# Kernel tuning notes

Measured on AMD Instinct MI355X. Metric: run time of the kernel, lower is better.

Reference implementation:

```python
import jax, jax.numpy as jnp
import numpy as np

B, N, C, F, E, K = 2, 2048, 1024, 4096, 8, 2

def setup_inputs() -> dict:
    key = jax.random.key(0)
    k = jax.random.split(key, 6)
    xavier1 = float(np.sqrt(6.0 / (C + F)))
    xavier2 = float(np.sqrt(6.0 / (F + C)))
    return {
        "x": jax.random.normal(k[0], (B, N, C), dtype=jnp.float32),
        "router_w": jax.random.normal(k[1], (E, C), dtype=jnp.float32) * 0.01,
        "w1": jax.random.uniform(k[2], (E, F, C), dtype=jnp.float32, minval=-xavier1, maxval=xavier1),
        "b1": jnp.zeros((E, F), dtype=jnp.float32),
        "w2": jax.random.uniform(k[3], (E, C, F), dtype=jnp.float32, minval=-xavier2, maxval=xavier2),
        "b2": jnp.zeros((E, C), dtype=jnp.float32),
    }

def reference(x, router_w, w1, b1, w2, b2):
    Bb, Nn, Cc = x.shape
    x_flat = x.reshape(-1, Cc)                                   # [T, C]
    # Router (eval mode: no noise)
    logits = jnp.einsum('tc,ec->te', x_flat, router_w)           # [T, E]
    probs = jax.nn.softmax(logits, axis=-1)
    top_w, top_idx = jax.lax.top_k(probs, K)                     # [T, K]
    top_w = top_w / (jnp.sum(top_w, axis=-1, keepdims=True) + 1e-9)
    # Dense all-expert MLP (same math as the per-expert gather/scatter loop)
    h = jnp.einsum('tc,efc->tef', x_flat, w1) + b1[None]          # [T, E, F]
    h = jax.nn.relu(h)
    y = jnp.einsum('tef,ecf->tec', h, w2) + b2[None]              # [T, E, C]
    # Gather the K selected experts per token and combine
    sel = jnp.take_along_axis(y, top_idx[:, :, None], axis=1)    # [T, K, C]
    out = jnp.einsum('tkc,tk->tc', sel, top_w)                   # [T, C]
    return out.reshape(Bb, Nn, Cc)
```

## Files before the change

kernel.cpp:

```cpp
#include <hip/hip_runtime.h>
#include <hip/hip_fp16.h>


#define T_TOK 4096
#define C_DIM 1024
#define F_DIM 4096
#define E_NUM 8
#define MAXT 80
#define NP   (MAXT * 128)
#define SUB_H 4096

typedef float f32x4 __attribute__((ext_vector_type(4)));
typedef _Float16 half8 __attribute__((ext_vector_type(8)));
typedef _Float16 half4 __attribute__((ext_vector_type(4)));

#define AS1 __attribute__((address_space(1)))
#define AS3 __attribute__((address_space(3)))

__device__ __forceinline__ half8 cvt8(float4 f0, float4 f1) {
  half8 hv;
  hv[0] = (_Float16)f0.x; hv[1] = (_Float16)f0.y; hv[2] = (_Float16)f0.z; hv[3] = (_Float16)f0.w;
  hv[4] = (_Float16)f1.x; hv[5] = (_Float16)f1.y; hv[6] = (_Float16)f1.z; hv[7] = (_Float16)f1.w;
  return hv;
}

__device__ __forceinline__ int xcd_swz(int bid, int nwg) {
  int xcd = bid & 7, rest = bid >> 3;
  int q = nwg >> 3, r = nwg & 7;
  return (xcd < r ? xcd * (q + 1) : r * (q + 1) + (xcd - r) * q) + rest;
}

__global__ __launch_bounds__(256) void router_kernel(
    const float* __restrict__ x, const float* __restrict__ rw,
    int* __restrict__ top_idx, float* __restrict__ top_w)
{
  int t = blockIdx.x * 4 + (threadIdx.x >> 6);
  int lane = threadIdx.x & 63;
  const float* xr = x + (size_t)t * C_DIM;
  float acc[E_NUM];
#pragma unroll
  for (int e = 0; e < E_NUM; ++e) acc[e] = 0.f;
  for (int j = 0; j < C_DIM / 64; ++j) {
    int c = j * 64 + lane;
    float xv = xr[c];
#pragma unroll
    for (int e = 0; e < E_NUM; ++e) acc[e] += xv * rw[e * C_DIM + c];
  }
#pragma unroll
  for (int e = 0; e < E_NUM; ++e) {
    float v = acc[e];
#pragma unroll
    for (int off = 32; off > 0; off >>= 1) v += __shfl_xor(v, off);
    acc[e] = v;
  }
  if (lane == 0) {
    float mx = acc[0];
    for (int e = 1; e < E_NUM; ++e) mx = fmaxf(mx, acc[e]);
    float p[E_NUM]; float Z = 0.f;
    for (int e = 0; e < E_NUM; ++e) { p[e] = expf(acc[e] - mx); Z += p[e]; }
    int b0 = 0;
    for (int e = 1; e < E_NUM; ++e) if (p[e] > p[b0]) b0 = e;
    int b1i = -1; float pb = -1.f;
    for (int e = 0; e < E_NUM; ++e) if (e != b0 && p[e] > pb) { pb = p[e]; b1i = e; }
    float p0 = p[b0] / Z, p1 = pb / Z;
    float s = p0 + p1 + 1e-9f;
    top_idx[t * 2 + 0] = b0;
    top_idx[t * 2 + 1] = b1i;
    top_w[t * 2 + 0] = p0 / s;
    top_w[t * 2 + 1] = p1 / s;
  }
}

__global__ void build_lists(const int* __restrict__ top_idx,
                            int* __restrict__ rows_g, int* __restrict__ counts,
                            int* __restrict__ tile_off, int* __restrict__ inv)
{
  int e = threadIdx.x >> 6;
  int lane = threadIdx.x & 63;
  int cnt = 0;
  for (int t0 = 0; t0 < T_TOK; t0 += 64) {
    int t = t0 + lane;
    bool sel = (top_idx[t * 2] == e) || (top_idx[t * 2 + 1] == e);
    cnt += __popcll(__ballot(sel));
  }
  if (lane == 0) counts[e] = cnt;
  __syncthreads();
  if (threadIdx.x == 0) {
    int o = 0;
    for (int i = 0; i < E_NUM; ++i) { tile_off[i] = o; o += 2 * ((counts[i] + 255) >> 8); }
    tile_off[E_NUM] = o;
  }
  __syncthreads();
  int base = tile_off[e] * 128;
  int pos = 0;
  for (int t0 = 0; t0 < T_TOK; t0 += 64) {
    int t = t0 + lane;
    int i0 = top_idx[t * 2], i1 = top_idx[t * 2 + 1];
    bool sel = (i0 == e) || (i1 == e);
    unsigned long long mask = __ballot(sel);
    if (sel) {
      int p = pos + __popcll(mask & ((1ull << lane) - 1ull));
      int slot = t * 2 + ((i0 == e) ? 0 : 1);
      rows_g[base + p] = slot;
      inv[slot] = (e << 16) | (base + p);
    }
    pos += __popcll(mask);
  }
}

__global__ __launch_bounds__(256) void gather_x(
    const float* __restrict__ x, const int* __restrict__ rows_g,
    const int* __restrict__ counts, const int* __restrict__ tile_off,
    _Float16* __restrict__ xg)
{
  unsigned g = blockIdx.x * 256 + threadIdx.x;
  unsigned p = g >> 7, ccr = g & 127;
  int gt = p >> 7, r = p & 127;
  int kc32 = ccr >> 2, c4d = ccr & 3;
  int c4s = c4d ^ (r & 3);
  int e = -1;
#pragma unroll
  for (int i = 0; i < E_NUM; ++i)
    if (gt >= tile_off[i] && gt < tile_off[i + 1]) e = i;
  half8 hv = {};
  if (e >= 0) {
    int nrem = counts[e] - (gt - tile_off[e]) * 128;
    if (r < nrem) {
      int t = rows_g[p] >> 1;
      const float4* s = reinterpret_cast<const float4*>(
          x + (size_t)t * C_DIM + kc32 * 32 + c4s * 8);
      hv = cvt8(s[0], s[1]);
    }
  }
  *reinterpret_cast<half8*>(xg + ((size_t)gt * 32 + kc32) * SUB_H + r * 32 + (c4d << 3)) = hv;
}

__global__ __launch_bounds__(256) void cvt_w(
    const float* __restrict__ w1, const float* __restrict__ w2,
    _Float16* __restrict__ w1t, _Float16* __restrict__ w2t,
    int ch, int Fc, int lgnftl, int lgnkc32, unsigned halfChunks)
{
  unsigned g = blockIdx.x * 256 + threadIdx.x;
  if (g < halfChunks) {
    unsigned tile = g >> 9;
    unsigned kc32 = tile & 31;
    unsigned et = tile >> 5;
    unsigned ftl = et & ((1u << lgnftl) - 1);
    unsigned e = et >> lgnftl;
    unsigned r = (g >> 2) & 127;
    unsigned sc = g & 3;
    unsigned c4s = sc ^ (r & 3);
    unsigned frow = ftl * 128 + r;
    const float4* s = reinterpret_cast<const float4*>(
        w1 + ((size_t)e * F_DIM + ch * Fc + frow) * C_DIM + kc32 * 32 + c4s * 8);
    *reinterpret_cast<half8*>(w1t + (size_t)g * 8) = cvt8(s[0], s[1]);
  } else {
    unsigned g2 = g - halfChunks;
    unsigned tile = g2 >> 9;
    unsigned kc32 = tile & ((1u << lgnkc32) - 1);
    unsigned et = tile >> lgnkc32;
    unsigned ct = et & 7;
    unsigned e = et >> 3;
    unsigned r = (g2 >> 2) & 127;
    unsigned sc = g2 & 3;
    unsigned c4s = sc ^ (r & 3);
    unsigned c = ct * 128 + r;
    const float4* s = reinterpret_cast<const float4*>(
        w2 + ((size_t)e * C_DIM + c) * F_DIM + ch * Fc + kc32 * 32 + c4s * 8);
    *reinterpret_cast<half8*>(w2t + (size_t)g2 * 8) = cvt8(s[0], s[1]);
  }
}

#define STAGE32(slot_, a0_, a1_, b0_, b1_)                                        \
  {                                                                               \
    int o_ = tid * 8;                                                             \
    __builtin_amdgcn_global_load_lds((const AS1 void*)((a0_) + o_),               \
        (AS3 void*)(lds + ((slot_) * 4 + 0) * SUB_H + o_), 16, 0, 0);             \
    __builtin_amdgcn_global_load_lds((const AS1 void*)((a1_) + o_),               \
        (AS3 void*)(lds + ((slot_) * 4 + 1) * SUB_H + o_), 16, 0, 0);             \
    __builtin_amdgcn_global_load_lds((const AS1 void*)((b0_) + o_),               \
        (AS3 void*)(lds + ((slot_) * 4 + 2) * SUB_H + o_), 16, 0, 0);             \
    __builtin_amdgcn_global_load_lds((const AS1 void*)((b1_) + o_),               \
        (AS3 void*)(lds + ((slot_) * 4 + 3) * SUB_H + o_), 16, 0, 0);             \
  }

#define COMPUTE32(slot_)                                                          \
  {                                                                               \
    const _Float16* aT_ = lds + (size_t)((slot_) * 4 + wr) * SUB_H;               \
    const _Float16* bT_ = lds + (size_t)((slot_) * 4 + 2 + (wc >> 1)) * SUB_H;    \
    const int c4_ = lane >> 4;                                                    \
    half8 aF[8], bF[4];                                                           \
    _Pragma("unroll")                                                             \
    for (int m = 0; m < 8; ++m) {                                                 \
      int r = m * 16 + (lane & 15);                                               \
      aF[m] = *reinterpret_cast<const half8*>(&aT_[r * 32 + ((c4_ ^ (r & 3)) << 3)]); \
    }                                                                             \
    _Pragma("unroll")                                                             \
    for (int n = 0; n < 4; ++n) {                                                 \
      int rb = (wc & 1) * 64 + n * 16 + (lane & 15);                              \
      bF[n] = *reinterpret_cast<const half8*>(&bT_[rb * 32 + ((c4_ ^ (rb & 3)) << 3)]); \
    }                                                                             \
    _Pragma("unroll")                                                             \
    for (int m = 0; m < 8; ++m)                                                   \
      _Pragma("unroll")                                                           \
      for (int n = 0; n < 4; ++n)                                                 \
        acc[m][n] = __builtin_amdgcn_mfma_f32_16x16x32_f16(bF[n], aF[m], acc[m][n], 0, 0, 0); \
  }

#define WAIT_BAR(cnt_)                                                            \
  asm volatile("s_waitcnt vmcnt(" #cnt_ ")" ::: "memory");                        \
  __builtin_amdgcn_sched_barrier(0);                                              \
  __builtin_amdgcn_s_barrier();                                                   \
  __builtin_amdgcn_sched_barrier(0);

#define KLOOP(n_)                                                                 \
  STAGE32(0, At0, At1, Bt0, Bt1);                                                 \
  STAGE32(1, At0 + SUB_H, At1 + SUB_H, Bt0 + SUB_H, Bt1 + SUB_H);                 \
  STAGE32(2, At0 + 2 * SUB_H, At1 + 2 * SUB_H, Bt0 + 2 * SUB_H, Bt1 + 2 * SUB_H); \
  for (int s = 0; s < (n_) - 2; ++s) {                                            \
    WAIT_BAR(8);                                                                  \
    COMPUTE32(s & 3);                                                             \
    if (s + 3 < (n_)) {                                                           \
      size_t ko_ = (size_t)(s + 3) * SUB_H;                                       \
      STAGE32((s + 3) & 3, At0 + ko_, At1 + ko_, Bt0 + ko_, Bt1 + ko_);           \
    }                                                                             \
  }                                                                               \
  WAIT_BAR(4);                                                                    \
  COMPUTE32(((n_) - 2) & 3);                                                      \
  WAIT_BAR(0);                                                                    \
  COMPUTE32(((n_) - 1) & 3);

__global__ __launch_bounds__(512, 2) void gemm1_kernel(
    const _Float16* __restrict__ xg, const _Float16* __restrict__ w1t,
    const float* __restrict__ b1, const int* __restrict__ tile_off,
    _Float16* __restrict__ ht, int ch, int Fc)
{
  extern __shared__ _Float16 lds[];
  const int NFT = Fc >> 8;
  const int GBf = (NFT < 4) ? NFT : 4;
  const int perg = 8 * GBf;
  const int ngrpF = NFT / GBf;
  const int wgid = xcd_swz(blockIdx.x, gridDim.x);
  const int grp = wgid / perg;
  const int inner = wgid - grp * perg;
  const int ftq = inner % GBf;
  const int gp = inner / GBf;
  const int gtg = grp / ngrpF;
  const int ftg = grp - gtg * ngrpF;
  const int ft = ftg * GBf + ftq;
  const int gt = (gtg * 8 + gp) * 2;
  if (gt >= tile_off[E_NUM]) return;
  int e = 0;
  while (gt >= tile_off[e + 1]) ++e;
  const int nftl = Fc >> 7;
  const _Float16* At0 = xg + (size_t)gt * 32 * SUB_H;
  const _Float16* At1 = xg + (size_t)(gt + 1) * 32 * SUB_H;
  const _Float16* Bt0 = w1t + (size_t)(e * nftl + 2 * ft) * 32 * SUB_H;
  const _Float16* Bt1 = w1t + (size_t)(e * nftl + 2 * ft + 1) * 32 * SUB_H;

  const int tid = threadIdx.x;
  const int lane = tid & 63;
  const int wave = tid >> 6;
  const int wr = wave >> 2, wc = wave & 3;

  f32x4 acc[8][4];
#pragma unroll
  for (int m = 0; m < 8; ++m)
#pragma unroll
    for (int n = 0; n < 4; ++n) acc[m][n] = (f32x4){0.f, 0.f, 0.f, 0.f};

  KLOOP(32);

  const int nkc32F = Fc >> 5;
  const int gtw = gt + wr;
  const float* b1e = b1 + e * F_DIM + ch * Fc;
#pragma unroll
  for (int m = 0; m < 8; ++m) {
    int tok = m * 16 + (lane & 15);
#pragma unroll
    for (int n = 0; n < 4; ++n) {
      int flb = ft * 256 + wc * 64 + n * 16 + ((lane >> 4) << 2);
      float4 bv = *reinterpret_cast<const float4*>(b1e + flb);
      half4 hv;
      hv[0] = (_Float16)fmaxf(acc[m][n][0] + bv.x, 0.f);
      hv[1] = (_Float16)fmaxf(acc[m][n][1] + bv.y, 0.f);
      hv[2] = (_Float16)fmaxf(acc[m][n][2] + bv.z, 0.f);
      hv[3] = (_Float16)fmaxf(acc[m][n][3] + bv.w, 0.f);
      *reinterpret_cast<half4*>(
          ht + ((size_t)gtw * nkc32F + (flb >> 5)) * SUB_H + tok * 32 +
          (((((flb >> 3) & 3) ^ (tok & 3))) << 3) + (flb & 7)) = hv;
    }
  }
}

__global__ __launch_bounds__(512, 2) void gemm2_kernel(
    const _Float16* __restrict__ ht, const _Float16* __restrict__ w2t,
    const int* __restrict__ tile_off, _Float16* __restrict__ y,
    int Fc, int kspl, int accum)
{
  extern __shared__ _Float16 lds[];
  const int NGT2 = MAXT / 2;
  const int wgid = xcd_swz(blockIdx.x, gridDim.x);
  const int ks = wgid / (NGT2 * 4);
  const int r0 = wgid - ks * NGT2 * 4;
  const int grp8 = r0 >> 5;
  const int inner = r0 & 31;
  const int ct2 = inner & 3;
  const int gp = inner >> 2;
  const int gt = (grp8 * 8 + gp) * 2;
  if (gt >= tile_off[E_NUM]) return;
  int e = 0;
  while (gt >= tile_off[e + 1]) ++e;
  const int nkc32 = Fc >> 5;
  const int klen = nkc32 / kspl;
  const _Float16* At0 = ht + ((size_t)gt * nkc32 + ks * klen) * SUB_H;
  const _Float16* At1 = ht + ((size_t)(gt + 1) * nkc32 + ks * klen) * SUB_H;
  const _Float16* Bt0 = w2t + ((size_t)(e * 8 + 2 * ct2) * nkc32 + ks * klen) * SUB_H;
  const _Float16* Bt1 = w2t + ((size_t)(e * 8 + 2 * ct2 + 1) * nkc32 + ks * klen) * SUB_H;

  const int tid = threadIdx.x;
  const int lane = tid & 63;
  const int wave = tid >> 6;
  const int wr = wave >> 2, wc = wave & 3;

  f32x4 acc[8][4];
#pragma unroll
  for (int m = 0; m < 8; ++m)
#pragma unroll
    for (int n = 0; n < 4; ++n) acc[m][n] = (f32x4){0.f, 0.f, 0.f, 0.f};

  KLOOP(klen);

  _Float16* yk = y + ((size_t)(ks * MAXT + gt + wr) * 128) * C_DIM;
#pragma unroll
  for (int m = 0; m < 8; ++m) {
    int tok = m * 16 + (lane & 15);
#pragma unroll
    for (int n = 0; n < 4; ++n) {
      int cb = ct2 * 256 + wc * 64 + n * 16 + ((lane >> 4) << 2);
      half4* p = reinterpret_cast<half4*>(yk + (size_t)tok * C_DIM + cb);
      half4 hv;
      if (accum) {
        half4 old = *p;
        hv[0] = (_Float16)(acc[m][n][0] + (float)old[0]);
        hv[1] = (_Float16)(acc[m][n][1] + (float)old[1]);
        hv[2] = (_Float16)(acc[m][n][2] + (float)old[2]);
        hv[3] = (_Float16)(acc[m][n][3] + (float)old[3]);
      } else {
        hv[0] = (_Float16)acc[m][n][0];
        hv[1] = (_Float16)acc[m][n][1];
        hv[2] = (_Float16)acc[m][n][2];
        hv[3] = (_Float16)acc[m][n][3];
      }
      *p = hv;
    }
  }
}

__global__ __launch_bounds__(256) void combine_kernel(
    const _Float16* __restrict__ y, const int* __restrict__ inv,
    const float* __restrict__ top_w, const float* __restrict__ b2,
    float* __restrict__ out, int kspl)
{
  int g = blockIdx.x * 256 + threadIdx.x;
  int t = g >> 7, c8 = (g & 127) << 3;
  float o[8];
#pragma unroll
  for (int i = 0; i < 8; ++i) o[i] = 0.f;
#pragma unroll
  for (int k = 0; k < 2; ++k) {
    int iv = inv[t * 2 + k];
    int e = iv >> 16, pos = iv & 0xffff;
    float w = top_w[t * 2 + k];
    const float4* bb = reinterpret_cast<const float4*>(b2 + e * C_DIM + c8);
    float4 bv0 = bb[0], bv1 = bb[1];
    float s[8] = {bv0.x, bv0.y, bv0.z, bv0.w, bv1.x, bv1.y, bv1.z, bv1.w};
    for (int ks = 0; ks < kspl; ++ks) {
      half8 hv = *reinterpret_cast<const half8*>(
          y + ((size_t)(ks * MAXT * 128 + pos)) * C_DIM + c8);
#pragma unroll
      for (int i = 0; i < 8; ++i) s[i] += (float)hv[i];
    }
#pragma unroll
    for (int i = 0; i < 8; ++i) o[i] += w * s[i];
  }
  float4* op = reinterpret_cast<float4*>(out + (size_t)t * C_DIM + c8);
  op[0] = (float4){o[0], o[1], o[2], o[3]};
  op[1] = (float4){o[4], o[5], o[6], o[7]};
}

extern "C" void kernel_launch(void* const* d_in, const int* in_sizes, int n_in,
                              void* d_out, int out_size, void* d_ws, size_t ws_size,
                              hipStream_t stream)
{
  const float* x  = (const float*)d_in[0];
  const float* rw = (const float*)d_in[1];
  const float* w1 = (const float*)d_in[2];
  const float* b1 = (const float*)d_in[3];
  const float* w2 = (const float*)d_in[4];
  const float* b2 = (const float*)d_in[5];
  float* out = (float*)d_out;

  char* ws = (char*)d_ws;
  size_t off = 0;
  auto carve = [&](size_t bytes) -> void* {
    void* p = ws + off;
    off += (bytes + 255) & ~(size_t)255;
    return p;
  };
  int*   top_idx  = (int*)carve((size_t)T_TOK * 2 * sizeof(int));
  float* top_w    = (float*)carve((size_t)T_TOK * 2 * sizeof(float));
  int*   counts   = (int*)carve(E_NUM * sizeof(int));
  int*   tile_off = (int*)carve((E_NUM + 1) * sizeof(int));
  int*   rows_g   = (int*)carve((size_t)NP * sizeof(int));
  int*   inv      = (int*)carve((size_t)T_TOK * 2 * sizeof(int));
  _Float16* xg    = (_Float16*)carve((size_t)MAXT * 32 * SUB_H * sizeof(_Float16));
  _Float16* y     = (_Float16*)carve((size_t)4 * NP * C_DIM * sizeof(_Float16));
  size_t fixed = off;

  int nchunk = 8;
  const int cands[4] = {1, 2, 4, 8};
  for (int ci = 0; ci < 4; ++ci) {
    int n = cands[ci];
    size_t fc = (size_t)(F_DIM / n);
    size_t w1b = ((size_t)E_NUM * fc * C_DIM * 2 + 255) & ~(size_t)255;
    size_t w2b = ((size_t)E_NUM * C_DIM * fc * 2 + 255) & ~(size_t)255;
    size_t htb = ((size_t)MAXT * (fc >> 5) * SUB_H * 2 + 255) & ~(size_t)255;
    if (fixed + w1b + w2b + htb <= ws_size) { nchunk = n; break; }
  }
  const int Fc = F_DIM / nchunk;
  int lgFc = 0; while ((1 << lgFc) < Fc) ++lgFc;
  _Float16* w1t = (_Float16*)carve((size_t)E_NUM * Fc * C_DIM * sizeof(_Float16));
  _Float16* w2t = (_Float16*)carve((size_t)E_NUM * C_DIM * Fc * sizeof(_Float16));
  _Float16* ht  = (_Float16*)carve((size_t)MAXT * (Fc >> 5) * SUB_H * sizeof(_Float16));

  const int kspl = (Fc >= 2048) ? 4 : 2;
  const size_t dynLds = (size_t)16 * SUB_H * sizeof(_Float16);

  router_kernel<<<T_TOK / 4, 256, 0, stream>>>(x, rw, top_idx, top_w);
  build_lists<<<1, 512, 0, stream>>>(top_idx, rows_g, counts, tile_off, inv);
  gather_x<<<(MAXT * 128 * 128) / 256, 256, 0, stream>>>(x, rows_g, counts, tile_off, xg);

  const unsigned halfChunks = (unsigned)Fc << 10;
  for (int ch = 0; ch < nchunk; ++ch) {
    cvt_w<<<8 * Fc, 256, 0, stream>>>(w1, w2, w1t, w2t, ch, Fc, lgFc - 7, lgFc - 5, halfChunks);
    gemm1_kernel<<<(MAXT / 2) * (Fc / 256), 512, dynLds, stream>>>(
        xg, w1t, b1, tile_off, ht, ch, Fc);
    gemm2_kernel<<<(MAXT / 2) * 4 * kspl, 512, dynLds, stream>>>(
        ht, w2t, tile_off, y, Fc, kspl, ch != 0);
  }
  combine_kernel<<<(T_TOK * 128) / 256, 256, 0, stream>>>(y, inv, top_w, b2, out, kspl);
}
```

Before: 358.7 us.

## Re-swizzle LDS tiles to 64-row XOR layout and split K-step into ping-pong halves

Changes the packed fp16 tile layout for activations, hidden states and weights from a 32-wide row with a 2-bit XOR swizzle to a 64-wide row with a 3-bit XOR swizzle, to cut LDS bank conflicts on fragment reads. Each K step of the GEMM main loop is now split into two halves that interleave LDS fragment reads, split global-to-LDS issues, and 16-MFMA groups run at raised wave priority, separated by extra barriers. The goal is better overlap of LDS reads with MFMA work and lower register pressure from holding only half the A fragments at a time. The cost is more barriers per K step. Every producer and consumer must agree on the new layout.

```diff
diff --git a/kernel.cpp b/kernel.cpp
--- a/kernel.cpp
+++ b/kernel.cpp
@@ -114,10 +114,9 @@
     _Float16* __restrict__ xg)
 {
   unsigned g = blockIdx.x * 256 + threadIdx.x;
-  unsigned p = g >> 7, ccr = g & 127;
+  unsigned p = g >> 7, c8g = g & 127;
   int gt = p >> 7, r = p & 127;
-  int kc32 = ccr >> 2, c4d = ccr & 3;
-  int c4s = c4d ^ (r & 3);
+  int ks32 = c8g >> 2, kidx = c8g & 3;
   int e = -1;
 #pragma unroll
   for (int i = 0; i < E_NUM; ++i)
@@ -128,107 +127,131 @@
     if (r < nrem) {
       int t = rows_g[p] >> 1;
       const float4* s = reinterpret_cast<const float4*>(
-          x + (size_t)t * C_DIM + kc32 * 32 + c4s * 8);
+          x + (size_t)t * C_DIM + ks32 * 32 + kidx * 8);
       hv = cvt8(s[0], s[1]);
     }
   }
-  *reinterpret_cast<half8*>(xg + ((size_t)gt * 32 + kc32) * SUB_H + r * 32 + (c4d << 3)) = hv;
+  int q = r & 63, h = r >> 6;
+  int slot = ((h << 2) | kidx) ^ (q & 7);
+  *reinterpret_cast<half8*>(
+      xg + ((size_t)gt * 32 + ks32) * SUB_H + q * 64 + slot * 8) = hv;
 }
 
 __global__ __launch_bounds__(256) void cvt_w(
     const float* __restrict__ w1, const float* __restrict__ w2,
     _Float16* __restrict__ w1t, _Float16* __restrict__ w2t,
-    int ch, int Fc, int lgnftl, int lgnkc32, unsigned halfChunks)
+    int ch, int Fc, int lgnftl, int lgnfs32, unsigned halfChunks)
 {
   unsigned g = blockIdx.x * 256 + threadIdx.x;
   if (g < halfChunks) {
     unsigned tile = g >> 9;
-    unsigned kc32 = tile & 31;
+    unsigned ks32 = tile & 31;
     unsigned et = tile >> 5;
     unsigned ftl = et & ((1u << lgnftl) - 1);
     unsigned e = et >> lgnftl;
-    unsigned r = (g >> 2) & 127;
-    unsigned sc = g & 3;
-    unsigned c4s = sc ^ (r & 3);
+    unsigned c = g & 511;
+    unsigned q = c >> 3, slot = c & 7;
+    unsigned sl = slot ^ (q & 7);
+    unsigned h = sl >> 2, kidx = sl & 3;
+    unsigned r = h * 64 + q;
     unsigned frow = ftl * 128 + r;
     const float4* s = reinterpret_cast<const float4*>(
-        w1 + ((size_t)e * F_DIM + ch * Fc + frow) * C_DIM + kc32 * 32 + c4s * 8);
+        w1 + ((size_t)e * F_DIM + ch * Fc + frow) * C_DIM + ks32 * 32 + kidx * 8);
     *reinterpret_cast<half8*>(w1t + (size_t)g * 8) = cvt8(s[0], s[1]);
   } else {
     unsigned g2 = g - halfChunks;
     unsigned tile = g2 >> 9;
-    unsigned kc32 = tile & ((1u << lgnkc32) - 1);
-    unsigned et = tile >> lgnkc32;
+    unsigned fs32 = tile & ((1u << lgnfs32) - 1);
+    unsigned et = tile >> lgnfs32;
     unsigned ct = et & 7;
     unsigned e = et >> 3;
-    unsigned r = (g2 >> 2) & 127;
-    unsigned sc = g2 & 3;
-    unsigned c4s = sc ^ (r & 3);
-    unsigned c = ct * 128 + r;
+    unsigned c = g2 & 511;
+    unsigned q = c >> 3, slot = c & 7;
+    unsigned sl = slot ^ (q & 7);
+    unsigned h = sl >> 2, kidx = sl & 3;
+    unsigned r = h * 64 + q;
+    unsigned crow = ct * 128 + r;
     const float4* s = reinterpret_cast<const float4*>(
-        w2 + ((size_t)e * C_DIM + c) * F_DIM + ch * Fc + kc32 * 32 + c4s * 8);
+        w2 + ((size_t)e * C_DIM + crow) * F_DIM + ch * Fc + fs32 * 32 + kidx * 8);
     *reinterpret_cast<half8*>(w2t + (size_t)g2 * 8) = cvt8(s[0], s[1]);
   }
 }
 
-#define STAGE32(slot_, a0_, a1_, b0_, b1_)                                        \
-  {                                                                               \
-    int o_ = tid * 8;                                                             \
-    __builtin_amdgcn_global_load_lds((const AS1 void*)((a0_) + o_),               \
-        (AS3 void*)(lds + ((slot_) * 4 + 0) * SUB_H + o_), 16, 0, 0);             \
-    __builtin_amdgcn_global_load_lds((const AS1 void*)((a1_) + o_),               \
-        (AS3 void*)(lds + ((slot_) * 4 + 1) * SUB_H + o_), 16, 0, 0);             \
-    __builtin_amdgcn_global_load_lds((const AS1 void*)((b0_) + o_),               \
-        (AS3 void*)(lds + ((slot_) * 4 + 2) * SUB_H + o_), 16, 0, 0);             \
-    __builtin_amdgcn_global_load_lds((const AS1 void*)((b1_) + o_),               \
-        (AS3 void*)(lds + ((slot_) * 4 + 3) * SUB_H + o_), 16, 0, 0);             \
-  }
-
-#define COMPUTE32(slot_)                                                          \
-  {                                                                               \
-    const _Float16* aT_ = lds + (size_t)((slot_) * 4 + wr) * SUB_H;               \
-    const _Float16* bT_ = lds + (size_t)((slot_) * 4 + 2 + (wc >> 1)) * SUB_H;    \
-    const int c4_ = lane >> 4;                                                    \
-    half8 aF[8], bF[4];                                                           \
-    _Pragma("unroll")                                                             \
-    for (int m = 0; m < 8; ++m) {                                                 \
-      int r = m * 16 + (lane & 15);                                               \
-      aF[m] = *reinterpret_cast<const half8*>(&aT_[r * 32 + ((c4_ ^ (r & 3)) << 3)]); \
-    }                                                                             \
-    _Pragma("unroll")                                                             \
-    for (int n = 0; n < 4; ++n) {                                                 \
-      int rb = (wc & 1) * 64 + n * 16 + (lane & 15);                              \
-      bF[n] = *reinterpret_cast<const half8*>(&bT_[rb * 32 + ((c4_ ^ (rb & 3)) << 3)]); \
-    }                                                                             \
-    _Pragma("unroll")                                                             \
-    for (int m = 0; m < 8; ++m)                                                   \
-      _Pragma("unroll")                                                           \
-      for (int n = 0; n < 4; ++n)                                                 \
-        acc[m][n] = __builtin_amdgcn_mfma_f32_16x16x32_f16(bF[n], aF[m], acc[m][n], 0, 0, 0); \
-  }
-
-#define WAIT_BAR(cnt_)                                                            \
-  asm volatile("s_waitcnt vmcnt(" #cnt_ ")" ::: "memory");                        \
-  __builtin_amdgcn_sched_barrier(0);                                              \
-  __builtin_amdgcn_s_barrier();                                                   \
-  __builtin_amdgcn_sched_barrier(0);
-
-#define KLOOP(n_)                                                                 \
-  STAGE32(0, At0, At1, Bt0, Bt1);                                                 \
-  STAGE32(1, At0 + SUB_H, At1 + SUB_H, Bt0 + SUB_H, Bt1 + SUB_H);                 \
-  STAGE32(2, At0 + 2 * SUB_H, At1 + 2 * SUB_H, Bt0 + 2 * SUB_H, Bt1 + 2 * SUB_H); \
-  for (int s = 0; s < (n_) - 2; ++s) {                                            \
-    WAIT_BAR(8);                                                                  \
-    COMPUTE32(s & 3);                                                             \
-    if (s + 3 < (n_)) {                                                           \
-      size_t ko_ = (size_t)(s + 3) * SUB_H;                                       \
-      STAGE32((s + 3) & 3, At0 + ko_, At1 + ko_, Bt0 + ko_, Bt1 + ko_);           \
-    }                                                                             \
-  }                                                                               \
-  WAIT_BAR(4);                                                                    \
-  COMPUTE32(((n_) - 2) & 3);                                                      \
-  WAIT_BAR(0);                                                                    \
-  COMPUTE32(((n_) - 1) & 3);
+#define SUBT(hs_, t_) (lds + (size_t)((((hs_) & 3) * 4 + (t_))) * SUB_H)
+
+#define ISSUE2(hs_, t0_, t1_, s0_, s1_)                                          \
+  {                                                                              \
+    int o_ = tid * 8;                                                            \
+    __builtin_amdgcn_global_load_lds((const AS1 void*)((s0_) + o_),              \
+        (AS3 void*)(SUBT(hs_, t0_) + o_), 16, 0, 0);                             \
+    __builtin_amdgcn_global_load_lds((const AS1 void*)((s1_) + o_),              \
+        (AS3 void*)(SUBT(hs_, t1_) + o_), 16, 0, 0);                             \
+  }
+
+#define READ_A(hs_, mlo_)                                                        \
+  {                                                                              \
+    const _Float16* aT_ = SUBT(hs_, wr);                                         \
+    _Pragma("unroll")                                                            \
+    for (int mm = 0; mm < 4; ++mm) {                                             \
+      int m_ = (mlo_) + mm;                                                      \
+      int q_ = ((m_ & 3) << 4) + l15;                                            \
+      int sl_ = ((((m_ >> 2) << 2) | kidx) ^ l7);                                \
+      aF[mm] = *reinterpret_cast<const half8*>(&aT_[q_ * 64 + sl_ * 8]);         \
+    }                                                                            \
+  }
+
+#define READ_B(hs_)                                                              \
+  {                                                                              \
+    const _Float16* bT_ = SUBT(hs_, 2 + (wc >> 1));                              \
+    const int slb_ = ((((wc & 1) << 2) | kidx) ^ l7);                            \
+    _Pragma("unroll")                                                            \
+    for (int n_ = 0; n_ < 4; ++n_) {                                             \
+      int q_ = (n_ << 4) + l15;                                                  \
+      bF[n_] = *reinterpret_cast<const half8*>(&bT_[q_ * 64 + slb_ * 8]);        \
+    }                                                                            \
+  }
+
+#define MFMA16(mlo_)                                                             \
+  __builtin_amdgcn_s_setprio(1);                                                 \
+  _Pragma("unroll")                                                              \
+  for (int mm = 0; mm < 4; ++mm)                                                 \
+    _Pragma("unroll")                                                            \
+    for (int n_ = 0; n_ < 4; ++n_)                                               \
+      acc[(mlo_) + mm][n_] = __builtin_amdgcn_mfma_f32_16x16x32_f16(             \
+          bF[n_], aF[mm], acc[(mlo_) + mm][n_], 0, 0, 0);                        \
+  __builtin_amdgcn_s_setprio(0);
+
+#define SB __builtin_amdgcn_sched_barrier(0)
+
+#define HALFSTEP(hs_, vm_, doIssue_)                                             \
+  {                                                                              \
+    asm volatile("s_waitcnt vmcnt(" vm_ ")" ::: "memory");                       \
+    SB; __builtin_amdgcn_s_barrier(); SB;                                        \
+    READ_A(hs_, 0); READ_B(hs_);                                                 \
+    if (doIssue_) ISSUE2((hs_) + 3, 0, 1, aSrc0 + (size_t)((hs_) + 3) * SUB_H,   \
+                         aSrc1 + (size_t)((hs_) + 3) * SUB_H);                   \
+    SB; __builtin_amdgcn_s_barrier();                                            \
+    asm volatile("s_waitcnt lgkmcnt(0)" ::: "memory"); SB;                       \
+    MFMA16(0);                                                                   \
+    SB; __builtin_amdgcn_s_barrier(); SB;                                        \
+    READ_A(hs_, 4);                                                              \
+    if (doIssue_) ISSUE2((hs_) + 3, 2, 3, bSrc0 + (size_t)((hs_) + 3) * SUB_H,   \
+                         bSrc1 + (size_t)((hs_) + 3) * SUB_H);                   \
+    SB; __builtin_amdgcn_s_barrier();                                            \
+    asm volatile("s_waitcnt lgkmcnt(0)" ::: "memory"); SB;                       \
+    MFMA16(4);                                                                   \
+    SB; __builtin_amdgcn_s_barrier(); SB;                                        \
+  }
+
+#define KLOOP(n_)                                                                \
+  ISSUE2(0, 0, 1, aSrc0, aSrc1); ISSUE2(0, 2, 3, bSrc0, bSrc1);                  \
+  ISSUE2(1, 0, 1, aSrc0 + SUB_H, aSrc1 + SUB_H);                                 \
+  ISSUE2(1, 2, 3, bSrc0 + SUB_H, bSrc1 + SUB_H);                                 \
+  ISSUE2(2, 0, 1, aSrc0 + 2 * SUB_H, aSrc1 + 2 * SUB_H);                         \
+  ISSUE2(2, 2, 3, bSrc0 + 2 * SUB_H, bSrc1 + 2 * SUB_H);                         \
+  for (int hs = 0; hs < (n_) - 2; ++hs) HALFSTEP(hs, "8", hs + 3 < (n_));        \
+  HALFSTEP((n_) - 2, "4", 0);                                                    \
+  HALFSTEP((n_) - 1, "0", 0);
 
 __global__ __launch_bounds__(512, 2) void gemm1_kernel(
     const _Float16* __restrict__ xg, const _Float16* __restrict__ w1t,
@@ -253,42 +276,46 @@
   int e = 0;
   while (gt >= tile_off[e + 1]) ++e;
   const int nftl = Fc >> 7;
-  const _Float16* At0 = xg + (size_t)gt * 32 * SUB_H;
-  const _Float16* At1 = xg + (size_t)(gt + 1) * 32 * SUB_H;
-  const _Float16* Bt0 = w1t + (size_t)(e * nftl + 2 * ft) * 32 * SUB_H;
-  const _Float16* Bt1 = w1t + (size_t)(e * nftl + 2 * ft + 1) * 32 * SUB_H;
+  const _Float16* aSrc0 = xg + (size_t)gt * 32 * SUB_H;
+  const _Float16* aSrc1 = xg + (size_t)(gt + 1) * 32 * SUB_H;
+  const _Float16* bSrc0 = w1t + (size_t)(e * nftl + 2 * ft) * 32 * SUB_H;
+  const _Float16* bSrc1 = w1t + (size_t)(e * nftl + 2 * ft + 1) * 32 * SUB_H;
 
   const int tid = threadIdx.x;
   const int lane = tid & 63;
   const int wave = tid >> 6;
   const int wr = wave >> 2, wc = wave & 3;
+  const int l15 = lane & 15, l7 = lane & 7, kidx = lane >> 4;
 
   f32x4 acc[8][4];
 #pragma unroll
   for (int m = 0; m < 8; ++m)
 #pragma unroll
     for (int n = 0; n < 4; ++n) acc[m][n] = (f32x4){0.f, 0.f, 0.f, 0.f};
+  half8 aF[4], bF[4];
 
   KLOOP(32);
 
-  const int nkc32F = Fc >> 5;
+  const int nfs32 = Fc >> 5;
   const int gtw = gt + wr;
   const float* b1e = b1 + e * F_DIM + ch * Fc;
 #pragma unroll
   for (int m = 0; m < 8; ++m) {
-    int tok = m * 16 + (lane & 15);
+    int tok = m * 16 + l15;
+    int q = tok & 63, h = tok >> 6;
 #pragma unroll
     for (int n = 0; n < 4; ++n) {
-      int flb = ft * 256 + wc * 64 + n * 16 + ((lane >> 4) << 2);
+      int flb = ft * 256 + wc * 64 + n * 16 + (kidx << 2);
       float4 bv = *reinterpret_cast<const float4*>(b1e + flb);
       half4 hv;
       hv[0] = (_Float16)fmaxf(acc[m][n][0] + bv.x, 0.f);
       hv[1] = (_Float16)fmaxf(acc[m][n][1] + bv.y, 0.f);
       hv[2] = (_Float16)fmaxf(acc[m][n][2] + bv.z, 0.f);
       hv[3] = (_Float16)fmaxf(acc[m][n][3] + bv.w, 0.f);
+      int fs32 = flb >> 5, kloc = flb & 31;
+      int slot = ((h << 2) | (kloc >> 3)) ^ (q & 7);
       *reinterpret_cast<half4*>(
-          ht + ((size_t)gtw * nkc32F + (flb >> 5)) * SUB_H + tok * 32 +
-          (((((flb >> 3) & 3) ^ (tok & 3))) << 3) + (flb & 7)) = hv;
+          ht + ((size_t)gtw * nfs32 + fs32) * SUB_H + q * 64 + slot * 8 + (kloc & 7)) = hv;
     }
   }
 }
@@ -313,31 +340,33 @@
   while (gt >= tile_off[e + 1]) ++e;
   const int nkc32 = Fc >> 5;
   const int klen = nkc32 / kspl;
-  const _Float16* At0 = ht + ((size_t)gt * nkc32 + ks * klen) * SUB_H;
-  const _Float16* At1 = ht + ((size_t)(gt + 1) * nkc32 + ks * klen) * SUB_H;
-  const _Float16* Bt0 = w2t + ((size_t)(e * 8 + 2 * ct2) * nkc32 + ks * klen) * SUB_H;
-  const _Float16* Bt1 = w2t + ((size_t)(e * 8 + 2 * ct2 + 1) * nkc32 + ks * klen) * SUB_H;
+  const _Float16* aSrc0 = ht + ((size_t)gt * nkc32 + ks * klen) * SUB_H;
+  const _Float16* aSrc1 = ht + ((size_t)(gt + 1) * nkc32 + ks * klen) * SUB_H;
+  const _Float16* bSrc0 = w2t + ((size_t)(e * 8 + 2 * ct2) * nkc32 + ks * klen) * SUB_H;
+  const _Float16* bSrc1 = w2t + ((size_t)(e * 8 + 2 * ct2 + 1) * nkc32 + ks * klen) * SUB_H;
 
   const int tid = threadIdx.x;
   const int lane = tid & 63;
   const int wave = tid >> 6;
   const int wr = wave >> 2, wc = wave & 3;
+  const int l15 = lane & 15, l7 = lane & 7, kidx = lane >> 4;
 
   f32x4 acc[8][4];
 #pragma unroll
   for (int m = 0; m < 8; ++m)
 #pragma unroll
     for (int n = 0; n < 4; ++n) acc[m][n] = (f32x4){0.f, 0.f, 0.f, 0.f};
+  half8 aF[4], bF[4];
 
   KLOOP(klen);
 
   _Float16* yk = y + ((size_t)(ks * MAXT + gt + wr) * 128) * C_DIM;
 #pragma unroll
   for (int m = 0; m < 8; ++m) {
-    int tok = m * 16 + (lane & 15);
+    int tok = m * 16 + l15;
 #pragma unroll
     for (int n = 0; n < 4; ++n) {
-      int cb = ct2 * 256 + wc * 64 + n * 16 + ((lane >> 4) << 2);
+      int cb = ct2 * 256 + wc * 64 + n * 16 + (kidx << 2);
       half4* p = reinterpret_cast<half4*>(yk + (size_t)tok * C_DIM + cb);
       half4 hv;
       if (accum) {
```

After: 368.6 us. 2.8% more time.
